# Performance work log

Hardware: AMD Instinct MI355X
Metric: run time of the kernel (lower is better)

Reference implementation:

```python
import jax, jax.numpy as jnp
import numpy as np

N_NODES = 100000
N_EDGES = 1600000
HIDDEN = 128


def setup_inputs() -> dict:
    key = jax.random.key(0)
    k1, k2, k3 = jax.random.split(key, 3)
    pos = jax.random.normal(k1, (N_NODES, 3), dtype=jnp.float32)
    edge_index = jax.random.randint(k2, (2, N_EDGES), 0, N_NODES, dtype=jnp.int64)
    vector_features = jax.random.normal(k3, (N_NODES, 3, HIDDEN), dtype=jnp.float32)
    return {"pos": pos, "edge_index": edge_index, "vector_features": vector_features}


def reference(pos, edge_index, vector_features):
    # pos: (N,3); edge_index: (2,E); vector_features: (N,3,H) (unused by original math)
    H = vector_features.shape[-1]
    n_nodes = pos.shape[0]
    row, col = edge_index[0], edge_index[1]

    edge_vec = pos[col] - pos[row]                                  # (E,3)
    edge_dist = jnp.linalg.norm(edge_vec, axis=-1, keepdims=True) + 1e-8
    unit_vec = edge_vec / edge_dist                                 # (E,3)

    # scatter-add of unit vectors to both endpoints
    direction_units = (jnp.zeros((n_nodes, 3), dtype=pos.dtype)
                       .at[row].add(unit_vec)
                       .at[col].add(-unit_vec))                     # (N,3)

    # sum over spatial dim of du*du -> squared norm, broadcast to hidden
    angular_info = jnp.broadcast_to(
        jnp.sum(direction_units * direction_units, axis=1, keepdims=True),
        (n_nodes, H))                                               # (N,H)

    # vectorized per-edge dihedral: project v_i, v_j off the edge direction
    v_i = direction_units[row]                                      # (E,3)
    v_j = direction_units[col]                                      # (E,3)
    dot_vi = jnp.sum(v_i * unit_vec, axis=-1, keepdims=True)
    dot_vj = jnp.sum(v_j * (-unit_vec), axis=-1, keepdims=True)
    w_ij = v_i - dot_vi * unit_vec
    w_ji = v_j - dot_vj * (-unit_vec)
    dihedral_val = jnp.sum(w_ij * w_ji, axis=-1, keepdims=True)     # (E,1)
    dihedral_info = jnp.broadcast_to(dihedral_val, (edge_index.shape[1], H))

    return (angular_info, dihedral_info, direction_units)
```

## Files before the change

kernel.cpp:

```cpp
#include <hip/hip_runtime.h>
#include <math.h>

#define N_NODES 100000
#define N_EDGES 1600000
#define HIDDEN 128

#define NBINS      256
#define BIN_NODES  391
#define BIN_CAP_MAX 14336
#define BIN_CAP_MIN 13056
#define CUR_STRIDE 32
#define A_THREADS  1024
#define A_EPT      8
#define A_EPB      (A_THREADS * A_EPT)
#define A_BLOCKS   ((N_EDGES + A_EPB - 1) / A_EPB)
#define B_THREADS  1024
#define NPAD       100096

#define FP_SCALE   4194304.0f
#define FP_INV     (1.0f / 4194304.0f)


typedef float vfloat4 __attribute__((ext_vector_type(4)));

__global__ __launch_bounds__(256) void prep_kernel(
    const float* __restrict__ pos,
    unsigned* __restrict__ cursors,
    float4* __restrict__ pos4)
{
    int gid = blockIdx.x * 256 + threadIdx.x;
    if (gid < NBINS) cursors[gid * CUR_STRIDE] = 0u;
    if (gid < N_NODES) {
        pos4[gid] = make_float4(pos[gid * 3 + 0], pos[gid * 3 + 1],
                                pos[gid * 3 + 2], 0.0f);
    }
}

__global__ __launch_bounds__(A_THREADS) void bin_edges_kernel(
    const int* __restrict__ eidx,
    unsigned* __restrict__ cursors,
    unsigned* __restrict__ region,
    int cap)
{
    __shared__ unsigned cnt[NBINS];
    __shared__ unsigned base[NBINS];
    if (threadIdx.x < NBINS) cnt[threadIdx.x] = 0u;
    __syncthreads();

    const int eb = blockIdx.x * A_EPB + threadIdx.x * 2;

    bool     val[A_EPT];
    unsigned r[A_EPT], c[A_EPT], br[A_EPT], bc[A_EPT], orow[A_EPT], ocol[A_EPT];

    #pragma unroll
    for (int k = 0; k < A_EPT; k += 2) {
        int e = eb + k * A_THREADS;
        bool v = (e < N_EDGES);
        val[k] = v; val[k + 1] = v;
        if (v) {
            int2 rr = *reinterpret_cast<const int2*>(eidx + e);
            int2 cc = *reinterpret_cast<const int2*>(eidx + N_EDGES + e);
            r[k] = (unsigned)rr.x; r[k + 1] = (unsigned)rr.y;
            c[k] = (unsigned)cc.x; c[k + 1] = (unsigned)cc.y;
        }
    }
    #pragma unroll
    for (int k = 0; k < A_EPT; ++k) {
        if (val[k]) {
            br[k] = r[k] / BIN_NODES;
            bc[k] = c[k] / BIN_NODES;
            orow[k] = atomicAdd(&cnt[br[k]], 1u);
            ocol[k] = atomicAdd(&cnt[bc[k]], 1u);
        }
    }
    __syncthreads();

    if (threadIdx.x < NBINS)
        base[threadIdx.x] =
            atomicAdd(&cursors[threadIdx.x * CUR_STRIDE], cnt[threadIdx.x]);
    __syncthreads();

    #pragma unroll
    for (int k = 0; k < A_EPT; ++k) {
        if (val[k]) {
            region[(size_t)br[k] * cap + base[br[k]] + orow[k]] =
                ((r[k] - br[k] * BIN_NODES) << 17) | c[k];
            region[(size_t)bc[k] * cap + base[bc[k]] + ocol[k]] =
                ((c[k] - bc[k] * BIN_NODES) << 17) | r[k];
        }
    }
}

__device__ __forceinline__ void proc_rec(unsigned rec,
                                         const float4* __restrict__ posLDS4,
                                         const float4* __restrict__ pos4,
                                         int* __restrict__ acc) {
    unsigned other = rec & 0x1FFFFu;
    unsigned local = rec >> 17;
    float4 s = posLDS4[local];
    float4 p = pos4[other];
    float dx = p.x - s.x;
    float dy = p.y - s.y;
    float dz = p.z - s.z;
    float inv = 1.0f / (sqrtf(dx * dx + dy * dy + dz * dz) + 1e-8f);
    atomicAdd(&acc[local * 3 + 0], __float2int_rn(dx * inv * FP_SCALE));
    atomicAdd(&acc[local * 3 + 1], __float2int_rn(dy * inv * FP_SCALE));
    atomicAdd(&acc[local * 3 + 2], __float2int_rn(dz * inv * FP_SCALE));
}

__global__ __launch_bounds__(B_THREADS) void accumulate_kernel(
    const float4* __restrict__ pos4,
    const unsigned* __restrict__ cursors,
    const unsigned* __restrict__ region,
    int cap,
    float* __restrict__ du,
    float* __restrict__ ang,
    float4* __restrict__ du4)
{
    __shared__ int    acc[BIN_NODES * 3];
    __shared__ float4 posLDS4[BIN_NODES];
    const unsigned b = blockIdx.x;
    const unsigned nodebase = b * BIN_NODES;
    const unsigned nloc = min((unsigned)BIN_NODES,
                              (unsigned)(N_NODES - nodebase));

    for (int i = threadIdx.x; i < BIN_NODES * 3; i += B_THREADS) acc[i] = 0;
    for (unsigned i = threadIdx.x; i < nloc; i += B_THREADS)
        posLDS4[i] = pos4[nodebase + i];
    __syncthreads();

    const unsigned n = cursors[b * CUR_STRIDE];
    const unsigned* __restrict__ reg = region + (size_t)b * cap;
    const unsigned n4 = n & ~3u;

    for (unsigned i = threadIdx.x * 4; i < n4; i += B_THREADS * 4) {
        uint4 rc = *reinterpret_cast<const uint4*>(reg + i);
        proc_rec(rc.x, posLDS4, pos4, acc);
        proc_rec(rc.y, posLDS4, pos4, acc);
        proc_rec(rc.z, posLDS4, pos4, acc);
        proc_rec(rc.w, posLDS4, pos4, acc);
    }
    for (unsigned i = n4 + threadIdx.x; i < n; i += B_THREADS)
        proc_rec(reg[i], posLDS4, pos4, acc);
    __syncthreads();

    for (unsigned i = threadIdx.x; i < nloc * 3; i += B_THREADS)
        du[(size_t)nodebase * 3 + i] = (float)acc[i] * FP_INV;

    for (unsigned i = threadIdx.x; i < nloc; i += B_THREADS) {
        float x = (float)acc[i * 3 + 0] * FP_INV;
        float y = (float)acc[i * 3 + 1] * FP_INV;
        float z = (float)acc[i * 3 + 2] * FP_INV;
        du4[nodebase + i] = make_float4(x, y, z, x * x + y * y + z * z);
    }

    for (unsigned j = threadIdx.x; j < nloc * 32; j += B_THREADS) {
        unsigned node = j >> 5, c4 = j & 31;
        float x = (float)acc[node * 3 + 0] * FP_INV;
        float y = (float)acc[node * 3 + 1] * FP_INV;
        float z = (float)acc[node * 3 + 2] * FP_INV;
        float a = x * x + y * y + z * z;
        vfloat4 v4 = {a, a, a, a};
        __builtin_nontemporal_store(v4,
            reinterpret_cast<vfloat4*>(ang + (size_t)(nodebase + node) * HIDDEN) + c4);
    }
}

__global__ __launch_bounds__(256) void dihedral_kernel(
    const float4* __restrict__ pos4,
    const float4* __restrict__ du4,
    const int* __restrict__ eidx,
    float* __restrict__ dih)
{
    __shared__ float vals[256];
    const int e0 = blockIdx.x * 256;
    const int e  = e0 + threadIdx.x;

    {
        int r = eidx[e];
        int c = eidx[N_EDGES + e];
        float4 pr = pos4[r];
        float4 pc = pos4[c];
        float4 vi = du4[r];
        float4 vj = du4[c];

        float dx = pc.x - pr.x, dy = pc.y - pr.y, dz = pc.z - pr.z;
        float inv = 1.0f / (sqrtf(dx * dx + dy * dy + dz * dz) + 1e-8f);
        float ux = dx * inv, uy = dy * inv, uz = dz * inv;

        float a  = vi.x * ux + vi.y * uy + vi.z * uz;
        float b  = vj.x * ux + vj.y * uy + vj.z * uz;
        float vv = vi.x * vj.x + vi.y * vj.y + vi.z * vj.z;
        float uu = ux * ux + uy * uy + uz * uz;

        vals[threadIdx.x] = vv - a * b * (2.0f - uu);
    }
    __syncthreads();

    vfloat4* out = reinterpret_cast<vfloat4*>(dih + (size_t)e0 * HIDDEN);
    #pragma unroll
    for (int it = 0; it < 32; ++it) {
        int i = it * 256 + threadIdx.x;
        float v = vals[i >> 5];
        vfloat4 v4 = {v, v, v, v};
        __builtin_nontemporal_store(v4, out + i);
    }
}

__global__ void zero_du_kernel(float* __restrict__ du, int n) {
    int i = blockIdx.x * blockDim.x + threadIdx.x;
    if (i < n) du[i] = 0.0f;
}

__global__ void edge_scatter_kernel(const float* __restrict__ pos,
                                    const int* __restrict__ eidx,
                                    float* __restrict__ du) {
    int e = blockIdx.x * blockDim.x + threadIdx.x;
    if (e >= N_EDGES) return;
    int r = eidx[e];
    int c = eidx[N_EDGES + e];
    float dx = pos[c * 3 + 0] - pos[r * 3 + 0];
    float dy = pos[c * 3 + 1] - pos[r * 3 + 1];
    float dz = pos[c * 3 + 2] - pos[r * 3 + 2];
    float inv = 1.0f / (sqrtf(dx * dx + dy * dy + dz * dz) + 1e-8f);
    float ux = dx * inv, uy = dy * inv, uz = dz * inv;
    unsafeAtomicAdd(&du[r * 3 + 0],  ux);
    unsafeAtomicAdd(&du[r * 3 + 1],  uy);
    unsafeAtomicAdd(&du[r * 3 + 2],  uz);
    unsafeAtomicAdd(&du[c * 3 + 0], -ux);
    unsafeAtomicAdd(&du[c * 3 + 1], -uy);
    unsafeAtomicAdd(&du[c * 3 + 2], -uz);
}

__global__ void angular_kernel(const float* __restrict__ du,
                               float* __restrict__ ang) {
    int gid = blockIdx.x * blockDim.x + threadIdx.x;
    int node = gid >> 5;
    int c4   = gid & 31;
    float x = du[node * 3 + 0];
    float y = du[node * 3 + 1];
    float z = du[node * 3 + 2];
    float a = x * x + y * y + z * z;
    vfloat4 v4 = {a, a, a, a};
    __builtin_nontemporal_store(v4,
        reinterpret_cast<vfloat4*>(ang + (size_t)node * HIDDEN) + c4);
}

__global__ __launch_bounds__(256) void dihedral_fallback_kernel(
    const float* __restrict__ pos,
    const int* __restrict__ eidx,
    const float* __restrict__ du,
    float* __restrict__ dih)
{
    __shared__ float vals[256];
    const int e0 = blockIdx.x * 256;
    const int e  = e0 + threadIdx.x;
    {
        int r = eidx[e];
        int c = eidx[N_EDGES + e];
        float dx = pos[c * 3 + 0] - pos[r * 3 + 0];
        float dy = pos[c * 3 + 1] - pos[r * 3 + 1];
        float dz = pos[c * 3 + 2] - pos[r * 3 + 2];
        float inv = 1.0f / (sqrtf(dx * dx + dy * dy + dz * dz) + 1e-8f);
        float ux = dx * inv, uy = dy * inv, uz = dz * inv;
        float vix = du[r * 3 + 0], viy = du[r * 3 + 1], viz = du[r * 3 + 2];
        float vjx = du[c * 3 + 0], vjy = du[c * 3 + 1], vjz = du[c * 3 + 2];
        float dvi = vix * ux + viy * uy + viz * uz;
        float dvj = -(vjx * ux + vjy * uy + vjz * uz);
        float wix = vix - dvi * ux, wiy = viy - dvi * uy, wiz = viz - dvi * uz;
        float wjx = vjx + dvj * ux, wjy = vjy + dvj * uy, wjz = vjz + dvj * uz;
        vals[threadIdx.x] = wix * wjx + wiy * wjy + wiz * wjz;
    }
    __syncthreads();
    vfloat4* out = reinterpret_cast<vfloat4*>(dih + (size_t)e0 * HIDDEN);
    #pragma unroll
    for (int it = 0; it < 32; ++it) {
        int i = it * 256 + threadIdx.x;
        float v = vals[i >> 5];
        vfloat4 v4 = {v, v, v, v};
        __builtin_nontemporal_store(v4, out + i);
    }
}

extern "C" void kernel_launch(void* const* d_in, const int* in_sizes, int n_in,
                              void* d_out, int out_size, void* d_ws, size_t ws_size,
                              hipStream_t stream) {
    const float* pos  = (const float*)d_in[0];
    const int*   eidx = (const int*)d_in[1];

    float* out = (float*)d_out;
    float* ang = out;
    float* dih = out + (size_t)N_NODES * HIDDEN;
    float* du  = dih + (size_t)N_EDGES * HIDDEN;

    const size_t curWords  = (size_t)NBINS * CUR_STRIDE;
    const size_t tblWords  = (size_t)NPAD * 4;
    const size_t wsWords   = ws_size / 4;

    int cap = 0;
    if (wsWords > curWords + 2 * tblWords) {
        size_t avail = (wsWords - curWords - 2 * tblWords) / NBINS;
        avail &= ~(size_t)255;
        cap = (int)(avail < BIN_CAP_MAX ? avail : BIN_CAP_MAX);
    }

    if (cap >= BIN_CAP_MIN) {
        unsigned* cursors = (unsigned*)d_ws;
        float4*   pos4    = (float4*)((unsigned*)d_ws + curWords);
        float4*   du4     = (float4*)((unsigned*)d_ws + curWords + tblWords);
        unsigned* region  = (unsigned*)d_ws + curWords + 2 * tblWords;

        prep_kernel<<<(N_NODES + 255) / 256, 256, 0, stream>>>(pos, cursors, pos4);
        bin_edges_kernel<<<A_BLOCKS, A_THREADS, 0, stream>>>(eidx, cursors,
                                                             region, cap);
        accumulate_kernel<<<NBINS, B_THREADS, 0, stream>>>(pos4, cursors, region,
                                                           cap, du, ang, du4);
        dihedral_kernel<<<N_EDGES / 256, 256, 0, stream>>>(pos4, du4, eidx, dih);
    } else {
        zero_du_kernel<<<(N_NODES * 3 + 255) / 256, 256, 0, stream>>>(du, N_NODES * 3);
        edge_scatter_kernel<<<(N_EDGES + 255) / 256, 256, 0, stream>>>(pos, eidx, du);
        angular_kernel<<<(N_NODES * 32) / 256, 256, 0, stream>>>(du, ang);
        dihedral_fallback_kernel<<<N_EDGES / 256, 256, 0, stream>>>(pos, eidx, du, dih);
    }
}
```

Measured before the change: 212.1 us.

## Split accumulate bins across two blocks and fold pos4 packing into binning

New measurement: 211.7 us (median of 2 runs). About the same (-0.2%).

```diff
diff --git a/kernel.cpp b/kernel.cpp
--- a/kernel.cpp
+++ b/kernel.cpp
@@ -7,6 +7,7 @@
 
 #define NBINS      256
 #define BIN_NODES  391
+#define HALF_NODES 196
 #define BIN_CAP_MAX 14336
 #define BIN_CAP_MIN 13056
 #define CUR_STRIDE 32
@@ -23,28 +24,28 @@
 
 typedef float vfloat4 __attribute__((ext_vector_type(4)));
 
-__global__ __launch_bounds__(256) void prep_kernel(
+__global__ void zero_cursors_kernel(unsigned* __restrict__ cur) {
+    cur[threadIdx.x * CUR_STRIDE] = 0u;
+}
+
+__global__ __launch_bounds__(A_THREADS) void bin_edges_kernel(
+    const int* __restrict__ eidx,
     const float* __restrict__ pos,
     unsigned* __restrict__ cursors,
-    float4* __restrict__ pos4)
-{
-    int gid = blockIdx.x * 256 + threadIdx.x;
-    if (gid < NBINS) cursors[gid * CUR_STRIDE] = 0u;
-    if (gid < N_NODES) {
-        pos4[gid] = make_float4(pos[gid * 3 + 0], pos[gid * 3 + 1],
-                                pos[gid * 3 + 2], 0.0f);
-    }
-}
-
-__global__ __launch_bounds__(A_THREADS) void bin_edges_kernel(
-    const int* __restrict__ eidx,
-    unsigned* __restrict__ cursors,
     unsigned* __restrict__ region,
+    float4* __restrict__ pos4,
     int cap)
 {
     __shared__ unsigned cnt[NBINS];
     __shared__ unsigned base[NBINS];
     if (threadIdx.x < NBINS) cnt[threadIdx.x] = 0u;
+
+    {
+        int gid = blockIdx.x * A_THREADS + threadIdx.x;
+        if (gid < N_NODES)
+            pos4[gid] = make_float4(pos[gid * 3 + 0], pos[gid * 3 + 1],
+                                    pos[gid * 3 + 2], 0.0f);
+    }
     __syncthreads();
 
     const int eb = blockIdx.x * A_EPB + threadIdx.x * 2;
@@ -91,21 +92,24 @@
     }
 }
 
-__device__ __forceinline__ void proc_rec(unsigned rec,
+__device__ __forceinline__ void proc_rec(unsigned rec, unsigned half,
                                          const float4* __restrict__ posLDS4,
                                          const float4* __restrict__ pos4,
                                          int* __restrict__ acc) {
+    unsigned local = rec >> 17;
+    unsigned h = (local >= HALF_NODES) ? 1u : 0u;
+    if (h != half) return;
+    unsigned l = local - half * HALF_NODES;
     unsigned other = rec & 0x1FFFFu;
-    unsigned local = rec >> 17;
-    float4 s = posLDS4[local];
+    float4 s = posLDS4[l];
     float4 p = pos4[other];
     float dx = p.x - s.x;
     float dy = p.y - s.y;
     float dz = p.z - s.z;
     float inv = 1.0f / (sqrtf(dx * dx + dy * dy + dz * dz) + 1e-8f);
-    atomicAdd(&acc[local * 3 + 0], __float2int_rn(dx * inv * FP_SCALE));
-    atomicAdd(&acc[local * 3 + 1], __float2int_rn(dy * inv * FP_SCALE));
-    atomicAdd(&acc[local * 3 + 2], __float2int_rn(dz * inv * FP_SCALE));
+    atomicAdd(&acc[l * 3 + 0], __float2int_rn(dx * inv * FP_SCALE));
+    atomicAdd(&acc[l * 3 + 1], __float2int_rn(dy * inv * FP_SCALE));
+    atomicAdd(&acc[l * 3 + 2], __float2int_rn(dz * inv * FP_SCALE));
 }
 
 __global__ __launch_bounds__(B_THREADS) void accumulate_kernel(
@@ -117,16 +121,18 @@
     float* __restrict__ ang,
     float4* __restrict__ du4)
 {
-    __shared__ int    acc[BIN_NODES * 3];
-    __shared__ float4 posLDS4[BIN_NODES];
-    const unsigned b = blockIdx.x;
-    const unsigned nodebase = b * BIN_NODES;
-    const unsigned nloc = min((unsigned)BIN_NODES,
-                              (unsigned)(N_NODES - nodebase));
-
-    for (int i = threadIdx.x; i < BIN_NODES * 3; i += B_THREADS) acc[i] = 0;
-    for (unsigned i = threadIdx.x; i < nloc; i += B_THREADS)
-        posLDS4[i] = pos4[nodebase + i];
+    __shared__ int    acc[HALF_NODES * 3];
+    __shared__ float4 posLDS4[HALF_NODES];
+    const unsigned b    = blockIdx.x >> 1;
+    const unsigned half = blockIdx.x & 1;
+    const unsigned g0   = b * BIN_NODES + half * HALF_NODES;
+    const int maxh = half ? (BIN_NODES - HALF_NODES) : HALF_NODES;
+    const int rem  = (int)N_NODES - (int)g0;
+    const unsigned nh = (unsigned)max(0, min(maxh, rem));
+
+    for (int i = threadIdx.x; i < HALF_NODES * 3; i += B_THREADS) acc[i] = 0;
+    for (unsigned i = threadIdx.x; i < nh; i += B_THREADS)
+        posLDS4[i] = pos4[g0 + i];
     __syncthreads();
 
     const unsigned n = cursors[b * CUR_STRIDE];
@@ -135,26 +141,26 @@
 
     for (unsigned i = threadIdx.x * 4; i < n4; i += B_THREADS * 4) {
         uint4 rc = *reinterpret_cast<const uint4*>(reg + i);
-        proc_rec(rc.x, posLDS4, pos4, acc);
-        proc_rec(rc.y, posLDS4, pos4, acc);
-        proc_rec(rc.z, posLDS4, pos4, acc);
-        proc_rec(rc.w, posLDS4, pos4, acc);
+        proc_rec(rc.x, half, posLDS4, pos4, acc);
+        proc_rec(rc.y, half, posLDS4, pos4, acc);
+        proc_rec(rc.z, half, posLDS4, pos4, acc);
+        proc_rec(rc.w, half, posLDS4, pos4, acc);
     }
     for (unsigned i = n4 + threadIdx.x; i < n; i += B_THREADS)
-        proc_rec(reg[i], posLDS4, pos4, acc);
-    __syncthreads();
-
-    for (unsigned i = threadIdx.x; i < nloc * 3; i += B_THREADS)
-        du[(size_t)nodebase * 3 + i] = (float)acc[i] * FP_INV;
-
-    for (unsigned i = threadIdx.x; i < nloc; i += B_THREADS) {
+        proc_rec(reg[i], half, posLDS4, pos4, acc);
+    __syncthreads();
+
+    for (unsigned i = threadIdx.x; i < nh * 3; i += B_THREADS)
+        du[(size_t)g0 * 3 + i] = (float)acc[i] * FP_INV;
+
+    for (unsigned i = threadIdx.x; i < nh; i += B_THREADS) {
         float x = (float)acc[i * 3 + 0] * FP_INV;
         float y = (float)acc[i * 3 + 1] * FP_INV;
         float z = (float)acc[i * 3 + 2] * FP_INV;
-        du4[nodebase + i] = make_float4(x, y, z, x * x + y * y + z * z);
-    }
-
-    for (unsigned j = threadIdx.x; j < nloc * 32; j += B_THREADS) {
+        du4[g0 + i] = make_float4(x, y, z, x * x + y * y + z * z);
+    }
+
+    for (unsigned j = threadIdx.x; j < nh * 32; j += B_THREADS) {
         unsigned node = j >> 5, c4 = j & 31;
         float x = (float)acc[node * 3 + 0] * FP_INV;
         float y = (float)acc[node * 3 + 1] * FP_INV;
@@ -162,7 +168,7 @@
         float a = x * x + y * y + z * z;
         vfloat4 v4 = {a, a, a, a};
         __builtin_nontemporal_store(v4,
-            reinterpret_cast<vfloat4*>(ang + (size_t)(nodebase + node) * HIDDEN) + c4);
+            reinterpret_cast<vfloat4*>(ang + (size_t)(g0 + node) * HIDDEN) + c4);
     }
 }
 
@@ -310,11 +316,12 @@
         float4*   du4     = (float4*)((unsigned*)d_ws + curWords + tblWords);
         unsigned* region  = (unsigned*)d_ws + curWords + 2 * tblWords;
 
-        prep_kernel<<<(N_NODES + 255) / 256, 256, 0, stream>>>(pos, cursors, pos4);
-        bin_edges_kernel<<<A_BLOCKS, A_THREADS, 0, stream>>>(eidx, cursors,
-                                                             region, cap);
-        accumulate_kernel<<<NBINS, B_THREADS, 0, stream>>>(pos4, cursors, region,
-                                                           cap, du, ang, du4);
+        zero_cursors_kernel<<<1, NBINS, 0, stream>>>(cursors);
+        bin_edges_kernel<<<A_BLOCKS, A_THREADS, 0, stream>>>(eidx, pos, cursors,
+                                                             region, pos4, cap);
+        accumulate_kernel<<<NBINS * 2, B_THREADS, 0, stream>>>(pos4, cursors,
+                                                               region, cap,
+                                                               du, ang, du4);
         dihedral_kernel<<<N_EDGES / 256, 256, 0, stream>>>(pos4, du4, eidx, dih);
     } else {
         zero_du_kernel<<<(N_NODES * 3 + 255) / 256, 256, 0, stream>>>(du, N_NODES * 3);
```
